# Performance work log

Measured on AMD Instinct MI355X. Metric: run time of the kernel, lower is better.

The kernel has to match this reference:

```python
import jax, jax.numpy as jnp
import numpy as np

D_MODEL = 256
D_K = 256
D_V = 256
B, S = 4, 4096


def setup_inputs() -> dict:
    key = jax.random.key(0)
    ks = jax.random.split(key, 9)
    q_in = jax.random.normal(ks[0], (B, S, D_MODEL), dtype=jnp.float32)
    k_in = jax.random.normal(ks[1], (B, S, D_MODEL), dtype=jnp.float32)
    v_in = jax.random.normal(ks[2], (B, S, D_MODEL), dtype=jnp.float32)
    # glorot-uniform-ish init for weights; biases small uniform (original uses glorot for bias too)
    lim_k = float(np.sqrt(6.0 / (D_MODEL + D_K)))
    lim_v = float(np.sqrt(6.0 / (D_MODEL + D_V)))
    Wq = jax.random.uniform(ks[3], (D_MODEL, D_K), minval=-lim_k, maxval=lim_k, dtype=jnp.float32)
    Wk = jax.random.uniform(ks[4], (D_MODEL, D_K), minval=-lim_k, maxval=lim_k, dtype=jnp.float32)
    Wv = jax.random.uniform(ks[5], (D_MODEL, D_V), minval=-lim_v, maxval=lim_v, dtype=jnp.float32)
    bq = jax.random.uniform(ks[6], (D_K,), minval=-lim_k, maxval=lim_k, dtype=jnp.float32)
    bk = jax.random.uniform(ks[7], (D_K,), minval=-lim_k, maxval=lim_k, dtype=jnp.float32)
    bv = jax.random.uniform(ks[8], (D_V,), minval=-lim_v, maxval=lim_v, dtype=jnp.float32)
    return {"q_in": q_in, "k_in": k_in, "v_in": v_in,
            "Wq": Wq, "bq": bq, "Wk": Wk, "bk": bk, "Wv": Wv, "bv": bv}


def reference(q_in, k_in, v_in, Wq, bq, Wk, bk, Wv, bv):
    # Dense projections on last dim
    q = jnp.einsum('bsd,dk->bsk', q_in, Wq) + bq  # [B,S,d_k]
    k = jnp.einsum('bsd,dk->bsk', k_in, Wk) + bk  # [B,S,d_k]
    v = jnp.einsum('bsd,dk->bsk', v_in, Wv) + bv  # [B,S,d_v]
    scale = 1.0 / jnp.sqrt(jnp.asarray(D_K, dtype=q.dtype))
    scores = jnp.einsum('bqk,bsk->bqs', q, k) * scale  # [B,S,S]
    attn = jax.nn.softmax(scores, axis=-1)
    return jnp.einsum('bqs,bsk->bqk', attn, v)  # [B,S,d_v]
```

## Files before the change

### kernel.cpp

```cpp
#include <hip/hip_runtime.h>
#include <hip/hip_bf16.h>
#include <stdint.h>

#define S_SZ 4096
#define SCL 0.09016844005586937f

typedef short bf16x8 __attribute__((ext_vector_type(8)));
typedef float f32x4 __attribute__((ext_vector_type(4)));
typedef float f32x16 __attribute__((ext_vector_type(16)));
typedef unsigned short u16;
typedef unsigned int u32;

#define MFMA16(a,b,c) __builtin_amdgcn_mfma_f32_16x16x32_bf16(a,b,c,0,0,0)
#define MFMA32(a,b,c) __builtin_amdgcn_mfma_f32_32x32x16_bf16(a,b,c,0,0,0)

__device__ __forceinline__ u32 cvtpk(float lo, float hi){
    u32 r;
    asm("v_cvt_pk_bf16_f32 %0, %1, %2" : "=v"(r) : "v"(lo), "v"(hi));
    return r;
}
__device__ __forceinline__ u16 cvt1(float a){ return (u16)cvtpk(a, a); }

__device__ __forceinline__ void async16(const void* g, void* l){
    __builtin_amdgcn_global_load_lds(
        (const __attribute__((address_space(1))) unsigned int*)g,
        (__attribute__((address_space(3))) unsigned int*)l, 16, 0, 0);
}

__global__ void wconv_kernel(const float* __restrict__ Wq, const float* __restrict__ Wk,
                             const float* __restrict__ Wv, u16* __restrict__ Wt){
    int idx = blockIdx.x*256 + threadIdx.x;
    int p = idx >> 16; int rem = idx & 65535;
    int dout = rem >> 8, din = rem & 255;
    const float* W = (p==0) ? Wq : ((p==1) ? Wk : Wv);
    Wt[idx] = cvt1(W[din*256 + dout]);
}

__global__ __launch_bounds__(512)
void proj_all_kernel(const float* __restrict__ Xq, const float* __restrict__ Xk,
                     const float* __restrict__ Xv, const u16* __restrict__ Wt,
                     const float* __restrict__ bq, const float* __restrict__ bk,
                     const float* __restrict__ bv,
                     u16* __restrict__ Qb, u16* __restrict__ Kb, u16* __restrict__ Vt){
    __shared__ char wlds[32768];
    int tid = threadIdx.x;
    int bid = blockIdx.x;
    int p = bid >> 7;
    const float* X    = (p==0) ? Xq : ((p==1) ? Xk : Xv);
    const float* bias = (p==0) ? bq : ((p==1) ? bk : bv);
    u16* Out          = (p==0) ? Qb : ((p==1) ? Kb : Vt);
    const char* Wbyte = (const char*)Wt + (size_t)p*131072;
    float scale = (p==0) ? SCL : 1.f;

    int w = tid >> 6, lane = tid & 63;
    int lr = lane & 15, lg = lane >> 4;
    int r0 = (bid & 127) * 128 + w * 16;

    bf16x8 a[8];
    #pragma unroll
    for (int ks = 0; ks < 8; ++ks){
        const float* src = X + (size_t)(r0 + lr)*256 + ks*32 + lg*8;
        float4 f0 = *(const float4*)src;
        float4 f1 = *(const float4*)(src+4);
        union { u32 wd[4]; bf16x8 v; } u;
        u.wd[0] = cvtpk(f0.x, f0.y);
        u.wd[1] = cvtpk(f0.z, f0.w);
        u.wd[2] = cvtpk(f1.x, f1.y);
        u.wd[3] = cvtpk(f1.z, f1.w);
        a[ks] = u.v;
    }

    for (int qtr = 0; qtr < 4; ++qtr){
        if (qtr) __syncthreads();
        const char* wsrc = Wbyte + qtr*32768;
        #pragma unroll
        for (int i = 0; i < 4; ++i){
            int o = i*8192 + tid*16;
            int dout = o >> 9, db = o & 511;
            async16(wsrc + ((dout<<9) | (db ^ ((dout&7)<<4))), wlds + o);
        }
        __syncthreads();

        #pragma unroll
        for (int dtl = 0; dtl < 4; ++dtl){
            int dt = qtr*4 + dtl;
            int dout_l = dtl*16 + lr;
            f32x4 acc = {0.f,0.f,0.f,0.f};
            #pragma unroll
            for (int ks = 0; ks < 8; ++ks){
                bf16x8 b = *(const bf16x8*)(wlds + dout_l*512 + ((ks*64 + lg*16) ^ ((dout_l&7)<<4)));
                acc = MFMA16(a[ks], b, acc);
            }
            float bv_ = bias[dt*16 + lr];
            int d = dt*16 + lr;
            if (p == 0){
                #pragma unroll
                for (int r = 0; r < 4; ++r){
                    int row = r0 + lg*4 + r;
                    Out[(size_t)row*256 + d] = cvt1((acc[r] + bv_)*scale);
                }
            } else if (p == 2){
                int row = r0 + lg*4;
                int bb = row >> 12;
                int s  = row & 4095;
                union { u32 wd[2]; ushort4 v; } u;
                u.wd[0] = cvtpk(acc[0]+bv_, acc[1]+bv_);
                u.wd[1] = cvtpk(acc[2]+bv_, acc[3]+bv_);
                u16* dst = Out + (size_t)bb*1048576 + (size_t)(s>>3)*2048 + d*8 + (s&7);
                *(ushort4*)dst = u.v;
            } else {
                int row = r0 + lg*4;
                int bb = row >> 12;
                int s  = row & 4095;
                u16* dst = Out + (size_t)bb*1048576 + (size_t)(d>>3)*32768 + (size_t)s*8 + (d&7);
                #pragma unroll
                for (int r = 0; r < 4; ++r)
                    dst[r*8] = cvt1(acc[r]+bv_);
            }
        }
    }
}

#define CH_ROWS 32
#define NCH     32

__global__ __launch_bounds__(512, 2)
void attn_kernel(const u16* __restrict__ Qb, const u16* __restrict__ Kb,
                 const u16* __restrict__ Vt, u16* __restrict__ Opart,
                 float* __restrict__ Mpart, float* __restrict__ Lpart){
    __shared__ char lds[131072];
    int tid = threadIdx.x;
    int w = tid >> 6, lane = tid & 63;
    int q5 = lane & 31, hi = lane >> 5;

    int bid = blockIdx.x;
    int xcd = bid & 7;
    int loc = bid >> 3;
    int combo = xcd*2 + (loc >> 4);
    int qb = loc & 15;
    int bb = combo >> 2;
    int split = combo & 3;
    int qrow0 = qb*256 + w*32;

    const char* Qbyte = (const char*)Qb + (size_t)bb*2097152;
    const char* Kbyte = (const char*)Kb + (size_t)bb*2097152;
    const char* Vbyte = (const char*)Vt + (size_t)bb*2097152;

    int kv0 = split*1024;

    auto STAGE = [&](int c){
        char* Kd = lds + (c&3)*16384;
        char* Vd = lds + 65536 + (c&3)*16384;
        int kv = kv0 + c*CH_ROWS;
        #pragma unroll
        for (int i = 0; i < 2; ++i){
            int o = i*8192 + tid*16;
            async16(Kbyte + ((size_t)(o>>9)*65536 + (size_t)kv*16 + (o&511)), Kd + o);
        }
        #pragma unroll
        for (int i = 0; i < 2; ++i){
            int o = i*8192 + tid*16;
            async16(Vbyte + (size_t)kv*512 + o, Vd + o);
        }
    };

    STAGE(0);
    STAGE(1);

    bf16x8 qf[16];
    #pragma unroll
    for (int c = 0; c < 16; ++c)
        qf[c] = *(const bf16x8*)(Qbyte + (size_t)(qrow0 + q5)*512 + c*32 + hi*16);
    asm volatile("s_waitcnt vmcnt(0)" ::: "memory");

    f32x16 acc[8];
    #pragma unroll
    for (int dt=0;dt<8;++dt)
        #pragma unroll
        for (int i=0;i<16;++i) acc[dt][i] = 0.f;
    float m = -1e30f, ls = 0.f;

    for (int ch = 0; ch < NCH; ++ch){
        if (ch + 2 < NCH) STAGE(ch + 2);
        if (ch < NCH-2)       { asm volatile("s_waitcnt vmcnt(8)" ::: "memory"); }
        else if (ch == NCH-2) { asm volatile("s_waitcnt vmcnt(4)" ::: "memory"); }
        else                  { asm volatile("s_waitcnt vmcnt(0)" ::: "memory"); }
        __builtin_amdgcn_sched_barrier(0);
        __builtin_amdgcn_s_barrier();
        __builtin_amdgcn_sched_barrier(0);

        char* Kl = lds + (ch&3)*16384;
        char* Vl = lds + 65536 + (ch&3)*16384;

        f32x16 sc;
        #pragma unroll
        for (int i=0;i<16;++i) sc[i] = 0.f;
        __builtin_amdgcn_s_setprio(1);
        #pragma unroll
        for (int c = 0; c < 16; ++c){
            bf16x8 kf = *(const bf16x8*)(Kl + (2*c + hi)*512 + q5*16);
            sc = MFMA32(kf, qf[c], sc);
        }
        __builtin_amdgcn_s_setprio(0);

        float x0 = fmaxf(sc[0], sc[1]),  x1 = fmaxf(sc[2], sc[3]);
        float x2 = fmaxf(sc[4], sc[5]),  x3 = fmaxf(sc[6], sc[7]);
        float x4 = fmaxf(sc[8], sc[9]),  x5 = fmaxf(sc[10], sc[11]);
        float x6 = fmaxf(sc[12], sc[13]),x7 = fmaxf(sc[14], sc[15]);
        float lmax = fmaxf(fmaxf(fmaxf(x0,x1), fmaxf(x2,x3)),
                           fmaxf(fmaxf(x4,x5), fmaxf(x6,x7)));
        float pm = fmaxf(lmax, __shfl_xor(lmax, 32));
        if (__any(pm > m + 8.0f)){
            float mn = fmaxf(m, pm);
            float alpha = __builtin_amdgcn_exp2f(m - mn);
            m = mn;
            ls *= alpha;
            #pragma unroll
            for (int dt=0;dt<8;++dt) acc[dt] *= alpha;
        }
        float p[16];
        #pragma unroll
        for (int i=0;i<16;++i) p[i] = __builtin_amdgcn_exp2f(sc[i] - m);
        ls += ((p[0]+p[1])+(p[2]+p[3])) + ((p[4]+p[5])+(p[6]+p[7]))
            + ((p[8]+p[9])+(p[10]+p[11])) + ((p[12]+p[13])+(p[14]+p[15]));

        bf16x8 pf0, pf1;
        {
            u32 A0 = cvtpk(p[0],p[1]), A1 = cvtpk(p[2],p[3]);
            u32 B0 = cvtpk(p[4],p[5]), B1 = cvtpk(p[6],p[7]);
            u32 XA0 = __shfl_xor(A0, 32), XA1 = __shfl_xor(A1, 32);
            u32 XB0 = __shfl_xor(B0, 32), XB1 = __shfl_xor(B1, 32);
            union { u32 wd[4]; bf16x8 v; } uu;
            uu.wd[0] = hi ? XB0 : A0;
            uu.wd[1] = hi ? XB1 : A1;
            uu.wd[2] = hi ? B0  : XA0;
            uu.wd[3] = hi ? B1  : XA1;
            pf0 = uu.v;
        }
        {
            u32 A0 = cvtpk(p[8],p[9]),   A1 = cvtpk(p[10],p[11]);
            u32 B0 = cvtpk(p[12],p[13]), B1 = cvtpk(p[14],p[15]);
            u32 XA0 = __shfl_xor(A0, 32), XA1 = __shfl_xor(A1, 32);
            u32 XB0 = __shfl_xor(B0, 32), XB1 = __shfl_xor(B1, 32);
            union { u32 wd[4]; bf16x8 v; } uu;
            uu.wd[0] = hi ? XB0 : A0;
            uu.wd[1] = hi ? XB1 : A1;
            uu.wd[2] = hi ? B0  : XA0;
            uu.wd[3] = hi ? B1  : XA1;
            pf1 = uu.v;
        }

        __builtin_amdgcn_s_setprio(1);
        #pragma unroll
        for (int dt=0; dt<8; ++dt){
            bf16x8 vf = *(const bf16x8*)(Vl + hi*4096 + (dt*32 + q5)*16);
            acc[dt] = MFMA32(vf, pf0, acc[dt]);
        }
        #pragma unroll
        for (int dt=0; dt<8; ++dt){
            bf16x8 vf = *(const bf16x8*)(Vl + (2 + hi)*4096 + (dt*32 + q5)*16);
            acc[dt] = MFMA32(vf, pf1, acc[dt]);
        }
        __builtin_amdgcn_s_setprio(0);
    }

    float l = ls + __shfl_xor(ls, 32);

    size_t pbase = (size_t)(split*4 + bb)*S_SZ*256;
    u16* orow = Opart + pbase + (size_t)(qrow0 + q5)*256;
    #pragma unroll
    for (int dt=0; dt<8; ++dt){
        #pragma unroll
        for (int g=0; g<4; ++g){
            int d0 = dt*32 + g*8 + hi*4;
            union { u32 wd[2]; uint2 v; } u2;
            u2.wd[0] = cvtpk(acc[dt][4*g+0], acc[dt][4*g+1]);
            u2.wd[1] = cvtpk(acc[dt][4*g+2], acc[dt][4*g+3]);
            *(uint2*)(orow + d0) = u2.v;
        }
    }
    if (lane < 32){
        int row = qrow0 + q5;
        Mpart[(split*4+bb)*S_SZ + row] = m;
        Lpart[(split*4+bb)*S_SZ + row] = l;
    }
}

__device__ __forceinline__ float bf2f(u16 x){
    union { u32 u; float f; } v; v.u = ((u32)x) << 16; return v.f;
}
__global__ void combine_kernel(const u16* __restrict__ Opart, const float* __restrict__ Mpart,
                               const float* __restrict__ Lpart, float* __restrict__ out){
    int idx = blockIdx.x*256 + threadIdx.x;
    int d4 = (idx & 63)*4;
    int row = idx >> 6;
    int bb = row >> 12, srow = row & 4095;
    float m[4], lv[4];
    #pragma unroll
    for (int i=0;i<4;++i){
        m[i]  = Mpart[(i*4+bb)*S_SZ + srow];
        lv[i] = Lpart[(i*4+bb)*S_SZ + srow];
    }
    float M = fmaxf(fmaxf(m[0],m[1]), fmaxf(m[2],m[3]));
    float L = 0.f; float wt[4];
    #pragma unroll
    for (int i=0;i<4;++i){ wt[i] = __builtin_amdgcn_exp2f(m[i]-M); L += lv[i]*wt[i]; }
    float inv = 1.f/L;
    float ox=0.f, oy=0.f, oz=0.f, ow=0.f;
    #pragma unroll
    for (int i=0;i<4;++i){
        ushort4 oi = *(const ushort4*)(Opart + (size_t)(i*4+bb)*S_SZ*256 + (size_t)srow*256 + d4);
        ox += bf2f(oi.x)*wt[i]; oy += bf2f(oi.y)*wt[i];
        oz += bf2f(oi.z)*wt[i]; ow += bf2f(oi.w)*wt[i];
    }
    float4 o; o.x = ox*inv; o.y = oy*inv; o.z = oz*inv; o.w = ow*inv;
    *(float4*)(out + (size_t)row*256 + d4) = o;
}

extern "C" void kernel_launch(void* const* d_in, const int* in_sizes, int n_in,
                              void* d_out, int out_size, void* d_ws, size_t ws_size,
                              hipStream_t stream) {
    const float* q_in = (const float*)d_in[0];
    const float* k_in = (const float*)d_in[1];
    const float* v_in = (const float*)d_in[2];
    const float* Wq   = (const float*)d_in[3];
    const float* bq   = (const float*)d_in[4];
    const float* Wk   = (const float*)d_in[5];
    const float* bk   = (const float*)d_in[6];
    const float* Wv   = (const float*)d_in[7];
    const float* bv   = (const float*)d_in[8];

    char* ws = (char*)d_ws;
    u16*  Qb    = (u16*)ws;
    u16*  Kb    = (u16*)(ws + 8388608);
    u16*  Vt    = (u16*)(ws + 16777216);
    u16*  Wt    = (u16*)(ws + 25165824);
    u16*  Opart = (u16*)(ws + 33554432);
    float* Mpart = (float*)(ws + 67108864);
    float* Lpart = (float*)(ws + 67371008);
    float* out   = (float*)d_out;

    hipLaunchKernelGGL(wconv_kernel,    dim3(768),  dim3(256), 0, stream, Wq, Wk, Wv, Wt);
    hipLaunchKernelGGL(proj_all_kernel, dim3(384),  dim3(512), 0, stream,
                       q_in, k_in, v_in, Wt, bq, bk, bv, Qb, Kb, Vt);
    hipLaunchKernelGGL(attn_kernel,     dim3(256),  dim3(512), 0, stream, Qb, Kb, Vt, Opart, Mpart, Lpart);
    hipLaunchKernelGGL(combine_kernel,  dim3(4096), dim3(256), 0, stream, Opart, Mpart, Lpart, out);
}
```

Baseline: 118.5 us.

## Double-buffer weight tiles in projection and widen combine per-thread work

The projection kernel now keeps two weight-tile LDS buffers. It prefetches the next quarter of the weights asynchronously while MFMAs run on the current one, which overlaps the load latency that the old single-buffer sync-load-sync loop exposed. The combine kernel now handles 8 output elements per thread instead of 4 and halves its grid, so per-row softmax-statistic loads are amortized over more elements. In exchange, LDS use in the projection kernel doubles to 64KB, which may limit occupancy.

```diff
diff --git a/kernel.cpp b/kernel.cpp
--- a/kernel.cpp
+++ b/kernel.cpp
@@ -42,7 +42,7 @@
                      const float* __restrict__ bq, const float* __restrict__ bk,
                      const float* __restrict__ bv,
                      u16* __restrict__ Qb, u16* __restrict__ Kb, u16* __restrict__ Vt){
-    __shared__ char wlds[32768];
+    __shared__ char wlds[65536];
     int tid = threadIdx.x;
     int bid = blockIdx.x;
     int p = bid >> 7;
@@ -55,6 +55,19 @@
     int w = tid >> 6, lane = tid & 63;
     int lr = lane & 15, lg = lane >> 4;
     int r0 = (bid & 127) * 128 + w * 16;
+
+    auto WSTAGE = [&](int q){
+        const char* wsrc = Wbyte + q*32768;
+        char* dst = wlds + (q&1)*32768;
+        #pragma unroll
+        for (int i = 0; i < 4; ++i){
+            int o = i*8192 + tid*16;
+            int dout = o >> 9, db = o & 511;
+            async16(wsrc + ((dout<<9) | (db ^ ((dout&7)<<4))), dst + o);
+        }
+    };
+
+    WSTAGE(0);
 
     bf16x8 a[8];
     #pragma unroll
@@ -69,17 +82,11 @@
         u.wd[3] = cvtpk(f1.z, f1.w);
         a[ks] = u.v;
     }
+    __syncthreads();
 
     for (int qtr = 0; qtr < 4; ++qtr){
-        if (qtr) __syncthreads();
-        const char* wsrc = Wbyte + qtr*32768;
-        #pragma unroll
-        for (int i = 0; i < 4; ++i){
-            int o = i*8192 + tid*16;
-            int dout = o >> 9, db = o & 511;
-            async16(wsrc + ((dout<<9) | (db ^ ((dout&7)<<4))), wlds + o);
-        }
-        __syncthreads();
+        if (qtr + 1 < 4) WSTAGE(qtr + 1);
+        const char* wb = wlds + (qtr&1)*32768;
 
         #pragma unroll
         for (int dtl = 0; dtl < 4; ++dtl){
@@ -88,7 +95,7 @@
             f32x4 acc = {0.f,0.f,0.f,0.f};
             #pragma unroll
             for (int ks = 0; ks < 8; ++ks){
-                bf16x8 b = *(const bf16x8*)(wlds + dout_l*512 + ((ks*64 + lg*16) ^ ((dout_l&7)<<4)));
+                bf16x8 b = *(const bf16x8*)(wb + dout_l*512 + ((ks*64 + lg*16) ^ ((dout_l&7)<<4)));
                 acc = MFMA16(a[ks], b, acc);
             }
             float bv_ = bias[dt*16 + lr];
@@ -118,6 +125,7 @@
                     dst[r*8] = cvt1(acc[r]+bv_);
             }
         }
+        __syncthreads();
     }
 }
 
@@ -292,8 +300,8 @@
 __global__ void combine_kernel(const u16* __restrict__ Opart, const float* __restrict__ Mpart,
                                const float* __restrict__ Lpart, float* __restrict__ out){
     int idx = blockIdx.x*256 + threadIdx.x;
-    int d4 = (idx & 63)*4;
-    int row = idx >> 6;
+    int d8 = (idx & 31)*8;
+    int row = idx >> 5;
     int bb = row >> 12, srow = row & 4095;
     float m[4], lv[4];
     #pragma unroll
@@ -306,15 +314,24 @@
     #pragma unroll
     for (int i=0;i<4;++i){ wt[i] = __builtin_amdgcn_exp2f(m[i]-M); L += lv[i]*wt[i]; }
     float inv = 1.f/L;
-    float ox=0.f, oy=0.f, oz=0.f, ow=0.f;
+    float o[8];
+    #pragma unroll
+    for (int j=0;j<8;++j) o[j] = 0.f;
     #pragma unroll
     for (int i=0;i<4;++i){
-        ushort4 oi = *(const ushort4*)(Opart + (size_t)(i*4+bb)*S_SZ*256 + (size_t)srow*256 + d4);
-        ox += bf2f(oi.x)*wt[i]; oy += bf2f(oi.y)*wt[i];
-        oz += bf2f(oi.z)*wt[i]; ow += bf2f(oi.w)*wt[i];
-    }
-    float4 o; o.x = ox*inv; o.y = oy*inv; o.z = oz*inv; o.w = ow*inv;
-    *(float4*)(out + (size_t)row*256 + d4) = o;
+        const u16* src = Opart + (size_t)(i*4+bb)*S_SZ*256 + (size_t)srow*256 + d8;
+        ushort4 lo = *(const ushort4*)src;
+        ushort4 hi4 = *(const ushort4*)(src + 4);
+        o[0] += bf2f(lo.x)*wt[i];  o[1] += bf2f(lo.y)*wt[i];
+        o[2] += bf2f(lo.z)*wt[i];  o[3] += bf2f(lo.w)*wt[i];
+        o[4] += bf2f(hi4.x)*wt[i]; o[5] += bf2f(hi4.y)*wt[i];
+        o[6] += bf2f(hi4.z)*wt[i]; o[7] += bf2f(hi4.w)*wt[i];
+    }
+    float* dst = out + (size_t)row*256 + d8;
+    float4 v0; v0.x = o[0]*inv; v0.y = o[1]*inv; v0.z = o[2]*inv; v0.w = o[3]*inv;
+    float4 v1; v1.x = o[4]*inv; v1.y = o[5]*inv; v1.z = o[6]*inv; v1.w = o[7]*inv;
+    *(float4*)dst = v0;
+    *(float4*)(dst + 4) = v1;
 }
 
 extern "C" void kernel_launch(void* const* d_in, const int* in_sizes, int n_in,
@@ -344,5 +361,5 @@
     hipLaunchKernelGGL(proj_all_kernel, dim3(384),  dim3(512), 0, stream,
                        q_in, k_in, v_in, Wt, bq, bk, bv, Qb, Kb, Vt);
     hipLaunchKernelGGL(attn_kernel,     dim3(256),  dim3(512), 0, stream, Qb, Kb, Vt, Opart, Mpart, Lpart);
-    hipLaunchKernelGGL(combine_kernel,  dim3(4096), dim3(256), 0, stream, Opart, Mpart, Lpart, out);
-}
+    hipLaunchKernelGGL(combine_kernel,  dim3(2048), dim3(256), 0, stream, Opart, Mpart, Lpart, out);
+}
```

Result: no change. 116.2 us (-1.9%).
